# Kernel optimization log

Measured on AMD Instinct MI355X. Metric: run time of the kernel, lower is better.

Reference implementation:

```python
import jax, jax.numpy as jnp
import numpy as np

B, S, E, H, L, V = 2, 2048, 512, 8, 4, 10000
D = E // H  # head_dim = 64


def _linear(x, W, b):
    # torch nn.Linear: y = x @ W.T + b, W: [out, in]
    return jnp.einsum('bse,oe->bso', x, W) + b


def _layernorm(x, g, b, eps=1e-5):
    mu = jnp.mean(x, axis=-1, keepdims=True)
    var = jnp.mean((x - mu) ** 2, axis=-1, keepdims=True)
    return (x - mu) * jax.lax.rsqrt(var + eps) * g + b


def _mha(x, Wq, bq, Wk, bk, Wv, bv, Wo, bo):
    q = _linear(x, Wq, bq).reshape(B, S, H, D).transpose(0, 2, 1, 3)
    k = _linear(x, Wk, bk).reshape(B, S, H, D).transpose(0, 2, 1, 3)
    v = _linear(x, Wv, bv).reshape(B, S, H, D).transpose(0, 2, 1, 3)
    energy = jnp.einsum('bhqd,bhkd->bhqk', q, k)  # full [B,H,S,S] scores (faithful)
    attn = jax.nn.softmax(energy / jnp.sqrt(jnp.asarray(D, x.dtype)), axis=-1)
    out = jnp.einsum('bhqk,bhkd->bhqd', attn, v)
    out = out.transpose(0, 2, 1, 3).reshape(B, S, E)
    return _linear(out, Wo, bo)


def setup_inputs() -> dict:
    key = jax.random.key(0)
    ks = jax.random.split(key, 12)
    s = 0.02
    f32 = jnp.float32
    return {
        'tokens': jax.random.randint(ks[0], (B, S), 0, V, dtype=jnp.int32),
        'embed_table': jax.random.normal(ks[1], (V, E), f32) * s,
        'pos_enc': jax.random.normal(ks[2], (1, S, E), f32) * s,
        'Wq': jax.random.normal(ks[3], (L, E, E), f32) * s,
        'bq': jnp.zeros((L, E), f32),
        'Wk': jax.random.normal(ks[4], (L, E, E), f32) * s,
        'bk': jnp.zeros((L, E), f32),
        'Wv': jax.random.normal(ks[5], (L, E, E), f32) * s,
        'bv': jnp.zeros((L, E), f32),
        'Wo': jax.random.normal(ks[6], (L, E, E), f32) * s,
        'bo': jnp.zeros((L, E), f32),
        'ln_g': jnp.ones((L, E), f32),
        'ln_b': jnp.zeros((L, E), f32),
        'Wout': jax.random.normal(ks[7], (V, E), f32) * s,
        'bout': jnp.zeros((V,), f32),
    }


def reference(tokens, embed_table, pos_enc, Wq, bq, Wk, bk, Wv, bv, Wo, bo, ln_g, ln_b, Wout, bout):
    x = embed_table[tokens] + pos_enc[:, :S, :]
    for l in range(L):
        a = _mha(x, Wq[l], bq[l], Wk[l], bk[l], Wv[l], bv[l], Wo[l], bo[l])
        x = _layernorm(x + a, ln_g[l], ln_b[l])
    # NOTE: original module defines feed_forward but never calls it in forward()
    return jnp.einsum('bse,ve->bsv', x, Wout) + bout
```

## Files before the change

kernel.cpp:

```cpp
#include <hip/hip_runtime.h>
#include <hip/hip_bf16.h>

#define Bc 2
#define Sc 2048
#define Ec 512
#define Hc 8
#define Lc 4
#define Vc 10000
#define Dc 64
#define Mc (Bc*Sc)
#define NPAD 10112

typedef __hip_bfloat16 bf16;
typedef __attribute__((ext_vector_type(8))) short frag_ab;
typedef __attribute__((ext_vector_type(4))) float frag_cd;

typedef __attribute__((address_space(3))) void lds_t;
typedef __attribute__((address_space(1))) void gm_t;
static __device__ __forceinline__ void gload16(const void* g, void* l) {
  __builtin_amdgcn_global_load_lds((const gm_t*)g, (lds_t*)l, 16, 0, 0);
}
static __device__ __forceinline__ frag_ab ldfrag(const bf16* p) {
  return *(const frag_ab*)p;
}

#define ROR16(x, n) __uint_as_float((unsigned)__builtin_amdgcn_update_dpp( \
    0, (int)__float_as_uint(x), 0x120 | (n), 0xf, 0xf, true))
static __device__ __forceinline__ float rmax16(float x) {
  x = fmaxf(x, ROR16(x, 8));
  x = fmaxf(x, ROR16(x, 4));
  x = fmaxf(x, ROR16(x, 2));
  x = fmaxf(x, ROR16(x, 1));
  return x;
}
static __device__ __forceinline__ float rsum16(float x) {
  x += ROR16(x, 8);
  x += ROR16(x, 4);
  x += ROR16(x, 2);
  x += ROR16(x, 1);
  return x;
}

#define NQKV (Lc*1536*512)
#define NO   (Lc*512*512)
#define NOUT (NPAD*512)
__global__ void convert_kernel(const float* __restrict__ Wq, const float* __restrict__ Wk,
                               const float* __restrict__ Wv, const float* __restrict__ Wo,
                               const float* __restrict__ Wout,
                               bf16* __restrict__ wqkv, bf16* __restrict__ wo,
                               bf16* __restrict__ wout) {
  long i4 = (long)(blockIdx.x * 256 + threadIdx.x) * 4;
  if (i4 >= NQKV + NO + NOUT) return;
  float4 v;
  bf16* dst;
  if (i4 < NQKV) {
    int row = (int)(i4 >> 9), colb = (int)(i4 & 511);
    int l = row / 1536, rr = row - l * 1536;
    int seg = rr >> 9, r = rr & 511;
    const float* src = (seg == 0 ? Wq : seg == 1 ? Wk : Wv) + (((long)(l * 512 + r)) << 9) + colb;
    v = *(const float4*)src;
    dst = wqkv + i4;
  } else if (i4 < NQKV + NO) {
    long j = i4 - NQKV;
    v = *(const float4*)(Wo + j);
    dst = wo + j;
  } else {
    long j = i4 - NQKV - NO;
    int row = (int)(j >> 9);
    if (row < Vc) v = *(const float4*)(Wout + j);
    else { v.x = 0.f; v.y = 0.f; v.z = 0.f; v.w = 0.f; }
    dst = wout + j;
  }
  union { bf16 h[4]; short4 s4; } u;
  u.h[0] = __float2bfloat16(v.x);
  u.h[1] = __float2bfloat16(v.y);
  u.h[2] = __float2bfloat16(v.z);
  u.h[3] = __float2bfloat16(v.w);
  *(short4*)dst = u.s4;
}

__global__ void embed_kernel(const int* __restrict__ tok, const float* __restrict__ emb,
                             const float* __restrict__ pos, float* __restrict__ x,
                             bf16* __restrict__ xb) {
  int i = blockIdx.x * 256 + threadIdx.x;
  int row = i >> 9, c = i & 511;
  int s = row & (Sc - 1);
  float v = emb[tok[row] * Ec + c] + pos[s * Ec + c];
  x[i] = v;
  xb[i] = __float2bfloat16(v);
}

template<int MODE>
__global__ __launch_bounds__(256)
void gemm_tile(const bf16* __restrict__ A, const bf16* __restrict__ W,
               const float* __restrict__ b0, const float* __restrict__ b1,
               const float* __restrict__ b2,
               void* __restrict__ o0, void* __restrict__ o1, void* __restrict__ o2) {
  __shared__ bf16 As[128 * 32];
  __shared__ bf16 Bs[128 * 32];
  const int t = threadIdx.x;
  const int lane = t & 63;
  const int wv = t >> 6;
  const int c = lane & 15, quad = lane >> 4;
  const int m0 = blockIdx.x * 128, n0 = blockIdx.y * 128;
  const int wm = (wv & 1) * 64, wn = (wv >> 1) * 64;
  frag_cd acc[4][4] = {};

  const int p0 = t, p1 = t + 256;
  const int r0 = p0 >> 2, g0 = (p0 & 3) ^ ((r0 >> 1) & 3);
  const int r1 = p1 >> 2, g1 = (p1 & 3) ^ ((r1 >> 1) & 3);
  const bf16* a0 = A + (m0 + r0) * Ec + g0 * 8;
  const bf16* a1 = A + (m0 + r1) * Ec + g1 * 8;
  const bf16* w0 = W + (n0 + r0) * Ec + g0 * 8;
  const bf16* w1 = W + (n0 + r1) * Ec + g1 * 8;

  const int sw8 = ((quad ^ ((c >> 1) & 3))) * 8;

  for (int k = 0; k < Ec; k += 32) {
    __syncthreads();
    gload16(a0 + k, As + p0 * 8);
    gload16(a1 + k, As + p1 * 8);
    gload16(w0 + k, Bs + p0 * 8);
    gload16(w1 + k, Bs + p1 * 8);
    __syncthreads();
    frag_ab af[4], bfr[4];
#pragma unroll
    for (int i = 0; i < 4; ++i)
      af[i] = *(const frag_ab*)(As + (wm + i * 16 + c) * 32 + sw8);
#pragma unroll
    for (int j = 0; j < 4; ++j)
      bfr[j] = *(const frag_ab*)(Bs + (wn + j * 16 + c) * 32 + sw8);
#pragma unroll
    for (int i = 0; i < 4; ++i)
#pragma unroll
      for (int j = 0; j < 4; ++j)
        acc[i][j] = __builtin_amdgcn_mfma_f32_16x16x32_bf16(af[i], bfr[j], acc[i][j], 0, 0, 0);
  }

#pragma unroll
  for (int j = 0; j < 4; ++j) {
    int gn = n0 + wn + j * 16 + c;
    if (MODE == 0) {
      int seg = gn >> 9, col = gn & 511;
      const float* bp = seg == 0 ? b0 : seg == 1 ? b1 : b2;
      float bias = bp[col];
      int hh = col >> 6, dd = col & 63;
#pragma unroll
      for (int i = 0; i < 4; ++i)
#pragma unroll
        for (int ii = 0; ii < 4; ++ii) {
          int gm = m0 + wm + i * 16 + quad * 4 + ii;
          int bb = gm >> 11, ss = gm & (Sc - 1);
          float v = acc[i][j][ii] + bias;
          if (seg == 0)
            ((bf16*)o0)[((((bb << 3) + hh) * Sc + ss) << 6) + dd] = __float2bfloat16(v);
          else if (seg == 1)
            ((bf16*)o1)[((((bb << 3) + hh) * Sc + ss) << 6) + dd] = __float2bfloat16(v);
          else
            ((bf16*)o2)[((((bb << 3) + hh) << 6) + dd) * Sc + ss] = __float2bfloat16(v);
        }
    } else if (MODE == 1) {
      float bias = b0[gn];
#pragma unroll
      for (int i = 0; i < 4; ++i)
#pragma unroll
        for (int ii = 0; ii < 4; ++ii) {
          int gm = m0 + wm + i * 16 + quad * 4 + ii;
          ((float*)o0)[((long)gm << 9) + gn] = acc[i][j][ii] + bias;
        }
    } else {
      if (gn < Vc) {
        float bias = b0[gn];
#pragma unroll
        for (int i = 0; i < 4; ++i)
#pragma unroll
          for (int ii = 0; ii < 4; ++ii) {
            int gm = m0 + wm + i * 16 + quad * 4 + ii;
            ((float*)o0)[(long)gm * Vc + gn] = acc[i][j][ii] + bias;
          }
      }
    }
  }
}

__global__ __launch_bounds__(256)
void attn_kernel(const bf16* __restrict__ Q, const bf16* __restrict__ Kb,
                 const bf16* __restrict__ Vt, bf16* __restrict__ O) {
  __shared__ bf16 Ks[2][64 * 64];
  __shared__ bf16 Vs[2][64 * 64];
  __shared__ bf16 Ps[4][2][16 * 64];
  const int t = threadIdx.x;
  const int lane = t & 63, wv = t >> 6;
  const int c = lane & 15, quad = lane >> 4;

  int wg = (blockIdx.x & 7) * 32 + (blockIdx.x >> 3);
  const int bh = wg >> 4;
  const int q0 = (wg & 15) * 128 + wv * 32;

  const bf16* kbase = Kb + (long)bh * Sc * Dc;
  const bf16* vbase = Vt + (long)bh * Dc * Sc;

  const int p0 = t, p1 = t + 256;
  const int row0 = (p0 >> 2) & 63, g40 = (p0 & 3) ^ ((row0 >> 1) & 3);
  const int row1 = (p1 >> 2) & 63, g41 = (p1 & 3) ^ ((row1 >> 1) & 3);
  const bf16* ksrc0 = kbase + row0 * Dc + 0 * 32 + g40 * 8;
  const bf16* ksrc1 = kbase + row1 * Dc + 1 * 32 + g41 * 8;
  const bf16* vsrc0 = vbase + row0 * Sc + 0 * 32 + g40 * 8;
  const bf16* vsrc1 = vbase + row1 * Sc + 1 * 32 + g41 * 8;

  const bf16* qpA = Q + ((long)bh * Sc + q0 + c) * Dc + quad * 8;
  frag_ab aq0A = ldfrag(qpA);
  frag_ab aq1A = ldfrag(qpA + 32);
  const bf16* qpB = qpA + 16 * Dc;
  frag_ab aq0B = ldfrag(qpB);
  frag_ab aq1B = ldfrag(qpB + 32);

  const int sw8 = (quad ^ ((c >> 1) & 3)) * 8;

  float mA[4], lAr[4], mB[4], lBr[4];
  frag_cd oA[4] = {}, oB[4] = {};
#pragma unroll
  for (int i = 0; i < 4; ++i) { mA[i] = -1e30f; mB[i] = -1e30f; lAr[i] = 0.f; lBr[i] = 0.f; }

  bf16* plA = Ps[wv][0];
  bf16* plB = Ps[wv][1];

  gload16(ksrc0, Ks[0] + p0 * 8);
  gload16(ksrc1, Ks[0] + p1 * 8);
  gload16(vsrc0, Vs[0] + p0 * 8);
  gload16(vsrc1, Vs[0] + p1 * 8);

  for (int tI = 0; tI < 32; ++tI) {
    const int cur = tI & 1;
    if (tI < 31) {
      const int k0 = (tI + 1) * 64;
      bf16* kd = Ks[cur ^ 1];
      bf16* vd = Vs[cur ^ 1];
      gload16(ksrc0 + k0 * Dc, kd + p0 * 8);
      gload16(ksrc1 + k0 * Dc, kd + p1 * 8);
      gload16(vsrc0 + k0, vd + p0 * 8);
      gload16(vsrc1 + k0, vd + p1 * 8);
      asm volatile("s_waitcnt vmcnt(4)" ::: "memory");
    } else {
      asm volatile("s_waitcnt vmcnt(0)" ::: "memory");
    }
    __builtin_amdgcn_s_barrier();
    asm volatile("" ::: "memory");

    const bf16* KsB = Ks[cur];
    const bf16* VsB = Vs[cur];

    frag_cd sA[4] = {}, sB[4] = {};
#pragma unroll
    for (int j = 0; j < 4; ++j) {
      frag_ab kb0 = ldfrag(KsB + (j * 16 + c) * 32 + sw8);
      frag_ab kb1 = ldfrag(KsB + 2048 + (j * 16 + c) * 32 + sw8);
      sA[j] = __builtin_amdgcn_mfma_f32_16x16x32_bf16(aq0A, kb0, sA[j], 0, 0, 0);
      sA[j] = __builtin_amdgcn_mfma_f32_16x16x32_bf16(aq1A, kb1, sA[j], 0, 0, 0);
      sB[j] = __builtin_amdgcn_mfma_f32_16x16x32_bf16(aq0B, kb0, sB[j], 0, 0, 0);
      sB[j] = __builtin_amdgcn_mfma_f32_16x16x32_bf16(aq1B, kb1, sB[j], 0, 0, 0);
    }

    float alA[4], alB[4];
#pragma unroll
    for (int i = 0; i < 4; ++i) {
      float sc0 = sA[0][i] * 0.125f, sc1 = sA[1][i] * 0.125f;
      float sc2 = sA[2][i] * 0.125f, sc3 = sA[3][i] * 0.125f;
      float mx = rmax16(fmaxf(fmaxf(sc0, sc1), fmaxf(sc2, sc3)));
      float mn = fmaxf(mA[i], mx);
      alA[i] = __expf(mA[i] - mn);
      float pe0 = __expf(sc0 - mn), pe1 = __expf(sc1 - mn);
      float pe2 = __expf(sc2 - mn), pe3 = __expf(sc3 - mn);
      float rs = rsum16(pe0 + pe1 + pe2 + pe3);
      lAr[i] = lAr[i] * alA[i] + rs;
      mA[i] = mn;
      int row = quad * 4 + i;
      plA[row * 64 + ((((c >> 3) + 0) ^ (row & 7)) << 3) + (c & 7)] = __float2bfloat16(pe0);
      plA[row * 64 + ((((c >> 3) + 2) ^ (row & 7)) << 3) + (c & 7)] = __float2bfloat16(pe1);
      plA[row * 64 + ((((c >> 3) + 4) ^ (row & 7)) << 3) + (c & 7)] = __float2bfloat16(pe2);
      plA[row * 64 + ((((c >> 3) + 6) ^ (row & 7)) << 3) + (c & 7)] = __float2bfloat16(pe3);
    }
#pragma unroll
    for (int i = 0; i < 4; ++i) {
      float sc0 = sB[0][i] * 0.125f, sc1 = sB[1][i] * 0.125f;
      float sc2 = sB[2][i] * 0.125f, sc3 = sB[3][i] * 0.125f;
      float mx = rmax16(fmaxf(fmaxf(sc0, sc1), fmaxf(sc2, sc3)));
      float mn = fmaxf(mB[i], mx);
      alB[i] = __expf(mB[i] - mn);
      float pe0 = __expf(sc0 - mn), pe1 = __expf(sc1 - mn);
      float pe2 = __expf(sc2 - mn), pe3 = __expf(sc3 - mn);
      float rs = rsum16(pe0 + pe1 + pe2 + pe3);
      lBr[i] = lBr[i] * alB[i] + rs;
      mB[i] = mn;
      int row = quad * 4 + i;
      plB[row * 64 + ((((c >> 3) + 0) ^ (row & 7)) << 3) + (c & 7)] = __float2bfloat16(pe0);
      plB[row * 64 + ((((c >> 3) + 2) ^ (row & 7)) << 3) + (c & 7)] = __float2bfloat16(pe1);
      plB[row * 64 + ((((c >> 3) + 4) ^ (row & 7)) << 3) + (c & 7)] = __float2bfloat16(pe2);
      plB[row * 64 + ((((c >> 3) + 6) ^ (row & 7)) << 3) + (c & 7)] = __float2bfloat16(pe3);
    }

#pragma unroll
    for (int td = 0; td < 4; ++td)
#pragma unroll
      for (int i = 0; i < 4; ++i) { oA[td][i] *= alA[i]; oB[td][i] *= alB[i]; }
#pragma unroll
    for (int kk = 0; kk < 2; ++kk) {
      frag_ab apA = ldfrag(plA + c * 64 + ((((kk << 2) + quad) ^ (c & 7)) << 3));
      frag_ab apB = ldfrag(plB + c * 64 + ((((kk << 2) + quad) ^ (c & 7)) << 3));
#pragma unroll
      for (int td = 0; td < 4; ++td) {
        frag_ab vb = ldfrag(VsB + kk * 2048 + (td * 16 + c) * 32 + sw8);
        oA[td] = __builtin_amdgcn_mfma_f32_16x16x32_bf16(apA, vb, oA[td], 0, 0, 0);
        oB[td] = __builtin_amdgcn_mfma_f32_16x16x32_bf16(apB, vb, oB[td], 0, 0, 0);
      }
    }

    asm volatile("" ::: "memory");
    __builtin_amdgcn_s_barrier();
  }

  const int bb = bh >> 3, hh = bh & 7;
#pragma unroll
  for (int i = 0; i < 4; ++i) {
    float invA = 1.f / lAr[i];
    float invB = 1.f / lBr[i];
    int ssA = q0 + quad * 4 + i;
    int ssB = ssA + 16;
#pragma unroll
    for (int td = 0; td < 4; ++td) {
      O[((long)bb * Sc + ssA) * Ec + hh * Dc + td * 16 + c] = __float2bfloat16(oA[td][i] * invA);
      O[((long)bb * Sc + ssB) * Ec + hh * Dc + td * 16 + c] = __float2bfloat16(oB[td][i] * invB);
    }
  }
}

__global__ void ln_kernel(const float* __restrict__ x, const float* __restrict__ a,
                          const float* __restrict__ g, const float* __restrict__ bb,
                          float* __restrict__ xo, bf16* __restrict__ xbo) {
  int lane = threadIdx.x & 63, wv = threadIdx.x >> 6;
  int row = blockIdx.x * 4 + wv;
  const float* xr = x + (long)row * Ec;
  const float* ar = a + (long)row * Ec;
  float v[8];
  float sum = 0.f;
#pragma unroll
  for (int j = 0; j < 8; ++j) {
    int c = lane + j * 64;
    v[j] = xr[c] + ar[c];
    sum += v[j];
  }
#pragma unroll
  for (int d = 1; d < 64; d <<= 1) sum += __shfl_xor(sum, d, 64);
  float mu = sum * (1.f / 512.f);
  float sq = 0.f;
#pragma unroll
  for (int j = 0; j < 8; ++j) { float t = v[j] - mu; sq += t * t; }
#pragma unroll
  for (int d = 1; d < 64; d <<= 1) sq += __shfl_xor(sq, d, 64);
  float rs = 1.f / sqrtf(sq * (1.f / 512.f) + 1e-5f);
#pragma unroll
  for (int j = 0; j < 8; ++j) {
    int c = lane + j * 64;
    float y = (v[j] - mu) * rs * g[c] + bb[c];
    xo[(long)row * Ec + c] = y;
    xbo[(long)row * Ec + c] = __float2bfloat16(y);
  }
}

extern "C" void kernel_launch(void* const* d_in, const int* in_sizes, int n_in,
                              void* d_out, int out_size, void* d_ws, size_t ws_size,
                              hipStream_t stream) {
  const int*   tokens = (const int*)d_in[0];
  const float* embed  = (const float*)d_in[1];
  const float* pos    = (const float*)d_in[2];
  const float* Wq     = (const float*)d_in[3];
  const float* bq     = (const float*)d_in[4];
  const float* Wk     = (const float*)d_in[5];
  const float* bk     = (const float*)d_in[6];
  const float* Wv     = (const float*)d_in[7];
  const float* bv     = (const float*)d_in[8];
  const float* Wo     = (const float*)d_in[9];
  const float* bo     = (const float*)d_in[10];
  const float* ln_g   = (const float*)d_in[11];
  const float* ln_b   = (const float*)d_in[12];
  const float* Wout   = (const float*)d_in[13];
  const float* bout   = (const float*)d_in[14];
  float* out = (float*)d_out;

  char* ws = (char*)d_ws;
  size_t off = 0;
  float* x_f    = (float*)(ws + off); off += (size_t)Mc * Ec * 4;
  bf16*  xb     = (bf16*)(ws + off);  off += (size_t)Mc * Ec * 2;
  float* a_f    = (float*)(ws + off); off += (size_t)Mc * Ec * 4;
  bf16*  qb     = (bf16*)(ws + off);  off += (size_t)Mc * Ec * 2;
  bf16*  kb     = (bf16*)(ws + off);  off += (size_t)Mc * Ec * 2;
  bf16*  vtb    = (bf16*)(ws + off);  off += (size_t)Mc * Ec * 2;
  bf16*  attnb  = (bf16*)(ws + off);  off += (size_t)Mc * Ec * 2;
  bf16*  wqkv_b = (bf16*)(ws + off);  off += (size_t)NQKV * 2;
  bf16*  wo_b   = (bf16*)(ws + off);  off += (size_t)NO * 2;
  bf16*  wout_b = (bf16*)(ws + off);  off += (size_t)NOUT * 2;

  int nconv = (NQKV + NO + NOUT) / 4;
  convert_kernel<<<(nconv + 255) / 256, 256, 0, stream>>>(Wq, Wk, Wv, Wo, Wout,
                                                          wqkv_b, wo_b, wout_b);

  embed_kernel<<<(Mc * Ec) / 256, 256, 0, stream>>>(tokens, embed, pos, x_f, xb);

  dim3 gqkv(Mc / 128, 1536 / 128);
  dim3 go(Mc / 128, Ec / 128);
  for (int l = 0; l < Lc; ++l) {
    const bf16* wqkv_l = wqkv_b + (size_t)l * 1536 * Ec;
    const bf16* wo_l   = wo_b + (size_t)l * Ec * Ec;
    gemm_tile<0><<<gqkv, 256, 0, stream>>>(xb, wqkv_l, bq + l * Ec, bk + l * Ec,
                                           bv + l * Ec, qb, kb, vtb);
    attn_kernel<<<Hc * Bc * (Sc / 128), 256, 0, stream>>>(qb, kb, vtb, attnb);
    gemm_tile<1><<<go, 256, 0, stream>>>(attnb, wo_l, bo + l * Ec, nullptr, nullptr,
                                         a_f, nullptr, nullptr);
    ln_kernel<<<Mc / 4, 256, 0, stream>>>(x_f, a_f, ln_g + l * Ec, ln_b + l * Ec,
                                          x_f, xb);
  }

  dim3 glog(Mc / 128, NPAD / 128);
  gemm_tile<2><<<glog, 256, 0, stream>>>(xb, wout_b, bout, nullptr, nullptr,
                                         out, nullptr, nullptr);
}
```

Baseline: 728.0 us.

## Split attention over two key halves with a separate softmax-combine kernel

Each attention block now processes only half of the key sequence, doubling the grid so more waves are resident per CU, and writes unnormalized fp32 partial outputs plus running max and sum. A new combine kernel merges the two halves with log-sum-exp rescaling and writes the bf16 result. Launch bounds request two blocks per CU. This trades extra global memory traffic and an extra launch per layer for better occupancy and latency hiding.

```diff
diff --git a/kernel.cpp b/kernel.cpp
--- a/kernel.cpp
+++ b/kernel.cpp
@@ -10,6 +10,7 @@
 #define Dc 64
 #define Mc (Bc*Sc)
 #define NPAD 10112
+#define NROWS (16*Sc)
 
 typedef __hip_bfloat16 bf16;
 typedef __attribute__((ext_vector_type(8))) short frag_ab;
@@ -183,9 +184,10 @@
   }
 }
 
-__global__ __launch_bounds__(256)
+__global__ __launch_bounds__(256, 2)
 void attn_kernel(const bf16* __restrict__ Q, const bf16* __restrict__ Kb,
-                 const bf16* __restrict__ Vt, bf16* __restrict__ O) {
+                 const bf16* __restrict__ Vt,
+                 float* __restrict__ Op, float* __restrict__ mp, float* __restrict__ lp) {
   __shared__ bf16 Ks[2][64 * 64];
   __shared__ bf16 Vs[2][64 * 64];
   __shared__ bf16 Ps[4][2][16 * 64];
@@ -193,12 +195,13 @@
   const int lane = t & 63, wv = t >> 6;
   const int c = lane & 15, quad = lane >> 4;
 
-  int wg = (blockIdx.x & 7) * 32 + (blockIdx.x >> 3);
-  const int bh = wg >> 4;
+  int wg = (blockIdx.x & 7) * 64 + (blockIdx.x >> 3);
+  const int bh = wg >> 5;
+  const int split = (wg >> 4) & 1;
   const int q0 = (wg & 15) * 128 + wv * 32;
 
-  const bf16* kbase = Kb + (long)bh * Sc * Dc;
-  const bf16* vbase = Vt + (long)bh * Dc * Sc;
+  const bf16* kbase = Kb + (long)bh * Sc * Dc + (long)(split << 10) * Dc;
+  const bf16* vbase = Vt + (long)bh * Dc * Sc + (split << 10);
 
   const int p0 = t, p1 = t + 256;
   const int row0 = (p0 >> 2) & 63, g40 = (p0 & 3) ^ ((row0 >> 1) & 3);
@@ -230,9 +233,9 @@
   gload16(vsrc0, Vs[0] + p0 * 8);
   gload16(vsrc1, Vs[0] + p1 * 8);
 
-  for (int tI = 0; tI < 32; ++tI) {
+  for (int tI = 0; tI < 16; ++tI) {
     const int cur = tI & 1;
-    if (tI < 31) {
+    if (tI < 15) {
       const int k0 = (tI + 1) * 64;
       bf16* kd = Ks[cur ^ 1];
       bf16* vd = Vs[cur ^ 1];
@@ -319,19 +322,36 @@
     __builtin_amdgcn_s_barrier();
   }
 
-  const int bb = bh >> 3, hh = bh & 7;
+  const long rbase = (long)split * NROWS + (long)bh * Sc + q0;
 #pragma unroll
   for (int i = 0; i < 4; ++i) {
-    float invA = 1.f / lAr[i];
-    float invB = 1.f / lBr[i];
-    int ssA = q0 + quad * 4 + i;
-    int ssB = ssA + 16;
+    long rA = rbase + quad * 4 + i;
+    long rB = rA + 16;
+    if (c == 0) {
+      mp[rA] = mA[i]; lp[rA] = lAr[i];
+      mp[rB] = mB[i]; lp[rB] = lBr[i];
+    }
 #pragma unroll
     for (int td = 0; td < 4; ++td) {
-      O[((long)bb * Sc + ssA) * Ec + hh * Dc + td * 16 + c] = __float2bfloat16(oA[td][i] * invA);
-      O[((long)bb * Sc + ssB) * Ec + hh * Dc + td * 16 + c] = __float2bfloat16(oB[td][i] * invB);
-    }
-  }
+      Op[rA * Dc + td * 16 + c] = oA[td][i];
+      Op[rB * Dc + td * 16 + c] = oB[td][i];
+    }
+  }
+}
+
+__global__ void combine_kernel(const float* __restrict__ Op, const float* __restrict__ mp,
+                               const float* __restrict__ lp, bf16* __restrict__ O) {
+  int t = blockIdx.x * 256 + threadIdx.x;
+  int d = t & 63, r = t >> 6;
+  int bh = r >> 11, ss = r & (Sc - 1);
+  float m1 = mp[r], m2 = mp[NROWS + r];
+  float l1 = lp[r], l2 = lp[NROWS + r];
+  float M = fmaxf(m1, m2);
+  float a1 = __expf(m1 - M), a2 = __expf(m2 - M);
+  float denom = l1 * a1 + l2 * a2;
+  float o = (Op[(long)r * Dc + d] * a1 + Op[(long)(NROWS + r) * Dc + d] * a2) / denom;
+  int bb = bh >> 3, hh = bh & 7;
+  O[((long)bb * Sc + ss) * Ec + hh * Dc + d] = __float2bfloat16(o);
 }
 
 __global__ void ln_kernel(const float* __restrict__ x, const float* __restrict__ a,
@@ -399,6 +419,9 @@
   bf16*  wqkv_b = (bf16*)(ws + off);  off += (size_t)NQKV * 2;
   bf16*  wo_b   = (bf16*)(ws + off);  off += (size_t)NO * 2;
   bf16*  wout_b = (bf16*)(ws + off);  off += (size_t)NOUT * 2;
+  float* op_f   = (float*)(ws + off); off += (size_t)2 * NROWS * Dc * 4;
+  float* mp_f   = (float*)(ws + off); off += (size_t)2 * NROWS * 4;
+  float* lp_f   = (float*)(ws + off); off += (size_t)2 * NROWS * 4;
 
   int nconv = (NQKV + NO + NOUT) / 4;
   convert_kernel<<<(nconv + 255) / 256, 256, 0, stream>>>(Wq, Wk, Wv, Wo, Wout,
@@ -413,7 +436,9 @@
     const bf16* wo_l   = wo_b + (size_t)l * Ec * Ec;
     gemm_tile<0><<<gqkv, 256, 0, stream>>>(xb, wqkv_l, bq + l * Ec, bk + l * Ec,
                                            bv + l * Ec, qb, kb, vtb);
-    attn_kernel<<<Hc * Bc * (Sc / 128), 256, 0, stream>>>(qb, kb, vtb, attnb);
+    attn_kernel<<<2 * Hc * Bc * (Sc / 128), 256, 0, stream>>>(qb, kb, vtb,
+                                                              op_f, mp_f, lp_f);
+    combine_kernel<<<(NROWS * Dc) / 256, 256, 0, stream>>>(op_f, mp_f, lp_f, attnb);
     gemm_tile<1><<<go, 256, 0, stream>>>(attnb, wo_l, bo + l * Ec, nullptr, nullptr,
                                          a_f, nullptr, nullptr);
     ln_kernel<<<Mc / 4, 256, 0, stream>>>(x_f, a_f, ln_g + l * Ec, ln_b + l * Ec,
```

Result: faster. 663.1 us (-8.9%).
